# Performance work log

Measured on AMD Instinct MI355X. Metric: run time of the kernel, lower is better.

The kernel has to match this reference:

```python
import jax, jax.numpy as jnp
import numpy as np

K = 20  # top-K neighbors per stock
SLOPE = 0.2  # LeakyReLU negative slope


def _gru_layer(x, Wih, Whh, bih, bhh):
    # x: [N, T, D]; PyTorch GRU gate order: r, z, n
    H = Whh.shape[1]
    def step(h, xt):
        gi = xt @ Wih.T + bih            # [N, 3H]
        gh = h @ Whh.T + bhh             # [N, 3H]
        ir, iz, inn = jnp.split(gi, 3, axis=1)
        hr, hz, hn = jnp.split(gh, 3, axis=1)
        r = jax.nn.sigmoid(ir + hr)
        z = jax.nn.sigmoid(iz + hz)
        n = jnp.tanh(inn + r * hn)
        h_new = (1.0 - z) * n + z * h
        return h_new, h_new
    h0 = jnp.zeros((x.shape[0], H), x.dtype)
    _, ys = jax.lax.scan(step, h0, jnp.swapaxes(x, 0, 1))
    return jnp.swapaxes(ys, 0, 1)        # [N, T, H]


def _cos_sim(x, y):
    # torch: xy / (||x|| ||y||^T), NaN (0/0) replaced by 0
    xy = x @ y.T
    xn = jnp.sqrt(jnp.sum(x * x, axis=1, keepdims=True))
    yn = jnp.sqrt(jnp.sum(y * y, axis=1, keepdims=True))
    denom = xn @ yn.T
    safe = jnp.where(denom == 0.0, 1.0, denom)
    return jnp.where(denom == 0.0, 0.0, xy / safe)


def setup_inputs() -> dict:
    key = jax.random.key(0)
    ks = jax.random.split(key, 20)
    N, T, F, H = 4096, 64, 32, 128
    def rn(k, shape, scale=0.1):
        return jax.random.normal(k, shape, dtype=jnp.float32) * scale
    b01 = lambda n: jnp.full((n,), 0.1, jnp.float32)
    return {
        'x': jax.random.normal(ks[0], (N, T, F), dtype=jnp.float32),
        'Wih0': rn(ks[1], (3 * H, F)), 'Whh0': rn(ks[2], (3 * H, H)),
        'bih0': rn(ks[3], (3 * H,)), 'bhh0': rn(ks[4], (3 * H,)),
        'Wih1': rn(ks[5], (3 * H, H)), 'Whh1': rn(ks[6], (3 * H, H)),
        'bih1': rn(ks[7], (3 * H,)), 'bhh1': rn(ks[8], (3 * H,)),
        'W_hc': rn(ks[9], (H, H)), 'b_hc': b01(H),
        'W_hs': rn(ks[10], (H, H)), 'b_hs': b01(H),
        'W_fore': rn(ks[11], (H, H)), 'b_fore': b01(H),
        'W_back': rn(ks[12], (H, H)), 'b_back': b01(H),
        'W_indi': rn(ks[13], (H, H)), 'b_indi': b01(H),
        'W_out': rn(ks[14], (1, H)), 'b_out': b01(1),
    }


def reference(x, Wih0, Whh0, bih0, bhh0, Wih1, Whh1, bih1, bhh1,
              W_hc, b_hc, W_hs, b_hs, W_fore, b_fore, W_back, b_back,
              W_indi, b_indi, W_out, b_out):
    lrelu = lambda v: jax.nn.leaky_relu(v, SLOPE)
    h = _gru_layer(x, Wih0, Whh0, bih0, bhh0)
    h = _gru_layer(h, Wih1, Whh1, bih1, bhh1)
    g = h[:, -1, :]                                   # [N, H] last-step GRU output
    N = g.shape[0]

    sim = _cos_sim(g, g)                              # [N, N]
    diag = jnp.diagonal(sim)
    sim_off = sim * (1.0 - jnp.eye(N, dtype=sim.dtype))

    # top-K (by |sim|) neighbor mask via scatter
    cols = jax.lax.top_k(jnp.abs(sim_off), K)[1]      # [N, K]
    rows = jnp.repeat(jnp.arange(N), K)
    mask = jnp.zeros((N, N), sim.dtype).at[rows, cols.reshape(-1)].set(1.0)

    tks = sim_off * mask
    col_nz = (jnp.sum(tks, axis=0) != 0).astype(sim.dtype)
    tks = tks + jnp.diag(col_nz * diag)

    # concept features; zero rows (empty concepts) are masked instead of filtered
    concept_raw = tks.T @ g                           # [N, H]
    valid = (jnp.sum(concept_raw, axis=1) != 0).astype(g.dtype)
    cf = lrelu(concept_raw @ W_hc.T + b_hc) * valid[:, None]

    attn = jax.nn.softmax(_cos_sim(g, cf), axis=0)    # softmax over stocks per concept
    hs = lrelu((attn @ cf) @ W_hs.T + b_hs)
    back = lrelu(hs @ W_back.T + b_back)
    fore = lrelu(hs @ W_fore.T + b_fore)
    indi = lrelu((g - back) @ W_indi.T + b_indi)
    pred = (fore + indi) @ W_out.T + b_out            # [N, 1]
    return pred.squeeze(-1)
```

## Files before the change

kernel.cpp:

```cpp
#include <hip/hip_runtime.h>


typedef float f32x4 __attribute__((ext_vector_type(4)));
typedef short s16x8 __attribute__((ext_vector_type(8)));
typedef unsigned short u16;
typedef unsigned long long u64;

#define DEVFN static __device__ __forceinline__

DEVFN u16 f2bf(float f) {
  union { float f; unsigned u; } v; v.f = f;
  return (u16)((v.u + 0x7FFFu + ((v.u >> 16) & 1u)) >> 16);
}

DEVFN f32x4 mfma16(s16x8 a, s16x8 b, f32x4 c) {
  return __builtin_amdgcn_mfma_f32_16x16x32_bf16(a, b, c, 0, 0, 0);
}

DEVFN float sigmf(float x) { return __builtin_amdgcn_rcpf(1.f + __expf(-x)); }
DEVFN float tanhf_fast(float x) {
  float e = __expf(2.f * x);
  return 1.f - 2.f * __builtin_amdgcn_rcpf(e + 1.f);
}
DEVFN float lrelu(float v) { return v > 0.f ? v : 0.2f * v; }

__global__ void cvt_all(const float* __restrict__ w0, const float* __restrict__ w1,
                        const float* __restrict__ w2, const float* __restrict__ w3,
                        const float* __restrict__ w4, const float* __restrict__ w5,
                        const float* __restrict__ w6, const float* __restrict__ w7,
                        u16* __restrict__ dst) {
  int i = blockIdx.x * 256 + threadIdx.x;
  if (i >= 225280) return;
  float v;
  if      (i < 12288)  v = w0[i];
  else if (i < 61440)  v = w1[i - 12288];
  else if (i < 110592) v = w2[i - 61440];
  else if (i < 159744) v = w3[i - 110592];
  else if (i < 176128) v = w4[i - 159744];
  else if (i < 192512) v = w5[i - 176128];
  else if (i < 208896) v = w6[i - 192512];
  else                 v = w7[i - 208896];
  dst[i] = f2bf(v);
}

template<int LAYER>
__launch_bounds__(512, 1)
__global__ void gru_kernel(const void* __restrict__ xin,
                           const u16* __restrict__ Wih, const u16* __restrict__ Whh,
                           const float* __restrict__ bih, const float* __restrict__ bhh,
                           u16* __restrict__ hseq_out, float* __restrict__ g_out)
{
  constexpr int KIN = (LAYER == 0) ? 32 : 128;
  constexpr int NKK = KIN / 32;
  constexpr int XS  = (LAYER == 0) ? 40 : 136;
  const int tid  = threadIdx.x;
  const int w    = tid >> 6;
  const int l    = tid & 63;
  const int quad = l >> 4;
  const int l16  = l & 15;
  const int r0   = blockIdx.x * 16;
  const int c    = w * 16 + l16;

  __shared__ u16 sh_x[16 * XS];
  __shared__ u16 sh_hb[16 * 136];

  s16x8 Bih[3][NKK];
  s16x8 Bhh[3][4];
  float bi[3], bh[3];
#pragma unroll
  for (int g = 0; g < 3; ++g) {
    int j = g * 128 + c;
    bi[g] = bih[j];
    bh[g] = bhh[j];
#pragma unroll
    for (int kk = 0; kk < NKK; ++kk)
      Bih[g][kk] = *(const s16x8*)(Wih + j * KIN + kk * 32 + quad * 8);
#pragma unroll
    for (int kk = 0; kk < 4; ++kk)
      Bhh[g][kk] = *(const s16x8*)(Whh + j * 128 + kk * 32 + quad * 8);
  }
  float hreg[4] = {0.f, 0.f, 0.f, 0.f};
  for (int idx = tid; idx < 16 * 136; idx += 512) sh_hb[idx] = 0;

  for (int t = 0; t < 64; ++t) {
    if constexpr (LAYER == 0) {
      int r = tid >> 5, cc = tid & 31;
      float xv = ((const float*)xin)[(size_t)(r0 + r) * (64 * 32) + t * 32 + cc];
      sh_x[r * XS + cc] = f2bf(xv);
    } else {
      int r = tid >> 5, c4 = (tid & 31) * 4;
      *(ushort4*)(sh_x + r * XS + c4) =
        *(const ushort4*)((const u16*)xin + (size_t)(r0 + r) * (64 * 128) + t * 128 + c4);
    }
    __syncthreads();
    s16x8 ax[NKK], ah[4];
#pragma unroll
    for (int kk = 0; kk < NKK; ++kk)
      ax[kk] = *(const s16x8*)(sh_x + l16 * XS + kk * 32 + quad * 8);
#pragma unroll
    for (int kk = 0; kk < 4; ++kk)
      ah[kk] = *(const s16x8*)(sh_hb + l16 * 136 + kk * 32 + quad * 8);
    __syncthreads();

    f32x4 ai[3], ahh[3];
    const f32x4 zz4 = {0.f, 0.f, 0.f, 0.f};
#pragma unroll
    for (int g = 0; g < 3; ++g) { ai[g] = zz4; ahh[g] = zz4; }
#pragma unroll
    for (int g = 0; g < 3; ++g)
#pragma unroll
      for (int kk = 0; kk < NKK; ++kk) ai[g] = mfma16(ax[kk], Bih[g][kk], ai[g]);
#pragma unroll
    for (int g = 0; g < 3; ++g)
#pragma unroll
      for (int kk = 0; kk < 4; ++kk)  ahh[g] = mfma16(ah[kk], Bhh[g][kk], ahh[g]);

#pragma unroll
    for (int i = 0; i < 4; ++i) {
      int m = quad * 4 + i;
      float rr = sigmf(ai[0][i] + bi[0] + ahh[0][i] + bh[0]);
      float zg = sigmf(ai[1][i] + bi[1] + ahh[1][i] + bh[1]);
      float nn = tanhf_fast(ai[2][i] + bi[2] + rr * (ahh[2][i] + bh[2]));
      float hnew = (1.f - zg) * nn + zg * hreg[i];
      hreg[i] = hnew;
      u16 hb = f2bf(hnew);
      sh_hb[m * 136 + c] = hb;
      if constexpr (LAYER == 0) {
        hseq_out[(size_t)(r0 + m) * (64 * 128) + t * 128 + c] = hb;
      } else {
        if (t == 63) g_out[(size_t)(r0 + m) * 128 + c] = hnew;
      }
    }
  }
}

__global__ void norm_cvt(const float* __restrict__ src, u16* __restrict__ dst,
                         float* __restrict__ rn)
{
  const int tid = threadIdx.x;
  const int wv = tid >> 6, l = tid & 63;
  const int row = blockIdx.x * 4 + wv;
  float2 f2 = *(const float2*)(src + (size_t)row * 128 + l * 2);
  float s = f2.x * f2.x + f2.y * f2.y;
#pragma unroll
  for (int off = 32; off >= 1; off >>= 1) s += __shfl_xor(s, off);
  ushort2 p; p.x = f2bf(f2.x); p.y = f2bf(f2.y);
  *(ushort2*)(dst + (size_t)row * 128 + l * 2) = p;
  if (l == 0) rn[row] = (s == 0.f) ? 0.f : rsqrtf(s);
}

template<int MODE>
__launch_bounds__(256, 1)
__global__ void cos_gemm(const u16* __restrict__ A, const u16* __restrict__ B,
                         const float* __restrict__ rnA, const float* __restrict__ rnB,
                         float* __restrict__ C, u16* __restrict__ E,
                         float* __restrict__ colsum)
{
  __shared__ u16 shA[128 * 136];
  __shared__ u16 shB[128 * 136];
  const int tid = threadIdx.x;
  const int l = tid & 63, wv = tid >> 6;
  const int quad = l >> 4, l16 = l & 15;
  const int i0 = blockIdx.y * 128, j0 = blockIdx.x * 128;
  {
    int r = tid >> 1, half = tid & 1;
    const int4* sa = (const int4*)(A + (size_t)(i0 + r) * 128 + half * 64);
    int4* da = (int4*)(shA + r * 136 + half * 64);
    const int4* sb = (const int4*)(B + (size_t)(j0 + r) * 128 + half * 64);
    int4* db = (int4*)(shB + r * 136 + half * 64);
#pragma unroll
    for (int q = 0; q < 8; ++q) { da[q] = sa[q]; db[q] = sb[q]; }
  }
  __syncthreads();
  const int wm = wv >> 1, wn = wv & 1;
  f32x4 acc[4][4];
  const f32x4 zz4 = {0.f, 0.f, 0.f, 0.f};
#pragma unroll
  for (int a = 0; a < 4; ++a)
#pragma unroll
    for (int b = 0; b < 4; ++b) acc[a][b] = zz4;
#pragma unroll
  for (int kk = 0; kk < 4; ++kk) {
    s16x8 af[4], bfr[4];
#pragma unroll
    for (int mt = 0; mt < 4; ++mt)
      af[mt] = *(const s16x8*)(shA + (wm * 64 + mt * 16 + l16) * 136 + kk * 32 + quad * 8);
#pragma unroll
    for (int nt = 0; nt < 4; ++nt)
      bfr[nt] = *(const s16x8*)(shB + (wn * 64 + nt * 16 + l16) * 136 + kk * 32 + quad * 8);
#pragma unroll
    for (int mt = 0; mt < 4; ++mt)
#pragma unroll
      for (int nt = 0; nt < 4; ++nt) acc[mt][nt] = mfma16(af[mt], bfr[nt], acc[mt][nt]);
  }
  float ra[4][4];
#pragma unroll
  for (int mt = 0; mt < 4; ++mt)
#pragma unroll
    for (int i = 0; i < 4; ++i) ra[mt][i] = rnA[i0 + wm * 64 + mt * 16 + quad * 4 + i];
#pragma unroll
  for (int nt = 0; nt < 4; ++nt) {
    int col = j0 + wn * 64 + nt * 16 + l16;
    float rb = rnB[col];
    float psum = 0.f;
#pragma unroll
    for (int mt = 0; mt < 4; ++mt)
#pragma unroll
      for (int i = 0; i < 4; ++i) {
        int row = i0 + wm * 64 + mt * 16 + quad * 4 + i;
        float v = acc[mt][nt][i] * ra[mt][i] * rb;
        if constexpr (MODE == 0) {
          C[(size_t)row * 4096 + col] = v;
        } else {
          float e = __expf(v);
          E[(size_t)row * 4096 + col] = f2bf(e);
          psum += e;
        }
      }
    if constexpr (MODE == 1) {
      psum += __shfl_xor(psum, 16);
      psum += __shfl_xor(psum, 32);
      if (quad == 0) atomicAdd(colsum + col, psum);
    }
  }
}

__launch_bounds__(256, 1)
__global__ void topk_select(const float* __restrict__ sim,
                            int* __restrict__ gselj, float* __restrict__ gselv,
                            int* __restrict__ cnt, int* __restrict__ touched)
{
  __shared__ unsigned hist[2048];
  __shared__ u64 cand[3072];
  __shared__ int selj[20];
  __shared__ unsigned ws4[4];
  __shared__ int shb, shcnt;
  const int tid = threadIdx.x;
  const int row = blockIdx.x;
  const int l = tid & 63, wv = tid >> 6;

  for (int i = tid; i < 2048; i += 256) hist[i] = 0;
  if (tid == 0) shcnt = 0;
  __syncthreads();

  unsigned key[4][4];
#pragma unroll
  for (int q = 0; q < 4; ++q) {
    int e0 = (q * 256 + tid) * 4;
    float4 v = *(const float4*)(sim + (size_t)row * 4096 + e0);
    key[q][0] = (e0 + 0 == row) ? 0u : (__float_as_uint(v.x) & 0x7FFFFFFFu);
    key[q][1] = (e0 + 1 == row) ? 0u : (__float_as_uint(v.y) & 0x7FFFFFFFu);
    key[q][2] = (e0 + 2 == row) ? 0u : (__float_as_uint(v.z) & 0x7FFFFFFFu);
    key[q][3] = (e0 + 3 == row) ? 0u : (__float_as_uint(v.w) & 0x7FFFFFFFu);
#pragma unroll
    for (int c = 0; c < 4; ++c) {
      unsigned bin = key[q][c] >> 19; if (bin > 2047u) bin = 2047u;
      atomicAdd(&hist[bin], 1u);
    }
  }
  __syncthreads();

  unsigned s = 0;
#pragma unroll
  for (int j = 0; j < 8; ++j) s += hist[tid * 8 + j];
  unsigned r = s;
#pragma unroll
  for (int off = 1; off < 64; off <<= 1) {
    unsigned o = __shfl_down(r, off);
    if (l + off < 64) r += o;
  }
  if (l == 0) ws4[wv] = r;
  __syncthreads();
  unsigned upper = 0;
  for (int q = wv + 1; q < 4; ++q) upper += ws4[q];
  unsigned excl = upper + (r - s);
  if (excl < 20u && excl + s >= 20u) {
    unsigned cum = excl;
    for (int j = 7; j >= 0; --j) {
      cum += hist[tid * 8 + j];
      if (cum >= 20u) { shb = tid * 8 + j; break; }
    }
  }
  __syncthreads();
  const unsigned b = (unsigned)shb;

#pragma unroll
  for (int q = 0; q < 4; ++q) {
    int e0 = (q * 256 + tid) * 4;
#pragma unroll
    for (int c = 0; c < 4; ++c) {
      unsigned bin = key[q][c] >> 19; if (bin > 2047u) bin = 2047u;
      if (bin >= b) {
        int p = atomicAdd(&shcnt, 1);
        if (p < 3072) cand[p] = ((u64)key[q][c] << 32) | (u64)(4095 - (e0 + c));
      }
    }
  }
  __syncthreads();
  const int C = (shcnt < 3072) ? shcnt : 3072;

  if (wv == 0) {
    for (int it = 0; it < 20; ++it) {
      u64 best = 0ull; int bpos = -1;
      for (int p = l; p < C; p += 64) {
        u64 cv = cand[p];
        if (cv > best) { best = cv; bpos = p; }
      }
      u64 mine = best;
#pragma unroll
      for (int off = 1; off < 64; off <<= 1) {
        u64 o = __shfl_xor(best, off);
        if (o > best) best = o;
      }
      if (mine == best && bpos >= 0 && best != 0ull) cand[bpos] = 0ull;
      if (l == 0) selj[it] = 4095 - (int)(best & 0xFFFull);
    }
  }
  __syncthreads();
  if (tid < 20) {
    int idx = selj[tid];
    float sv = (idx == row) ? 0.f : sim[(size_t)row * 4096 + idx];
    gselj[row * 20 + tid] = idx;
    gselv[row * 20 + tid] = sv;
    atomicAdd(&cnt[idx], 1);
    if (sv != 0.f) atomicOr(touched + idx, 1);
  }
}

__launch_bounds__(1024, 1)
__global__ void scan4096(const int* __restrict__ cnt, int* __restrict__ offs,
                         int* __restrict__ cur)
{
  __shared__ int wsum[16];
  const int t = threadIdx.x, l = t & 63, wv = t >> 6;
  int4 c = ((const int4*)cnt)[t];
  int s = c.x + c.y + c.z + c.w;
  int ps = s;
#pragma unroll
  for (int off = 1; off < 64; off <<= 1) {
    int o = __shfl_up(ps, off);
    if (l >= off) ps += o;
  }
  if (l == 63) wsum[wv] = ps;
  __syncthreads();
  if (t == 0) {
    int a = 0;
#pragma unroll
    for (int q = 0; q < 16; ++q) { int x = wsum[q]; wsum[q] = a; a += x; }
  }
  __syncthreads();
  int base = wsum[wv] + (ps - s);
  int4 o4;
  o4.x = base; o4.y = o4.x + c.x; o4.z = o4.y + c.y; o4.w = o4.z + c.z;
  ((int4*)offs)[t] = o4;
  ((int4*)cur)[t] = o4;
}

__global__ void scatter_entries(const int* __restrict__ gselj, const float* __restrict__ gselv,
                                int* __restrict__ cur, int* __restrict__ eid,
                                float* __restrict__ ev)
{
  unsigned idx = blockIdx.x * 256 + threadIdx.x;
  unsigned row = idx / 20u;
  int j = gselj[idx]; float v = gselv[idx];
  int pos = atomicAdd(&cur[j], 1);
  eid[pos] = (int)row; ev[pos] = v;
}

__launch_bounds__(128, 1)
__global__ void concept_cf(const int* __restrict__ offs, const int* __restrict__ cnt,
                           const int* __restrict__ eid, const float* __restrict__ ev,
                           const float* __restrict__ g, const float* __restrict__ sim,
                           const int* __restrict__ touched,
                           const float* __restrict__ Whc, const float* __restrict__ bhc,
                           float* __restrict__ cf, u16* __restrict__ cfbf,
                           float* __restrict__ rncf)
{
  __shared__ float shc[128];
  __shared__ float red2[2];
  const int j = blockIdx.x, d = threadIdx.x;
  const int l = d & 63, wv = d >> 6;
  const int off = offs[j], n = cnt[j];
  float acc = 0.f;
  for (int p = 0; p < n; ++p) {
    int i = eid[off + p]; float v = ev[off + p];
    acc += v * g[(size_t)i * 128 + d];
  }
  if (touched[j]) acc += sim[(size_t)j * 4097] * g[(size_t)j * 128 + d];
  float s = acc;
#pragma unroll
  for (int o = 32; o >= 1; o >>= 1) s += __shfl_xor(s, o);
  if (l == 0) red2[wv] = s;
  shc[d] = acc;
  __syncthreads();
  float valid = ((red2[0] + red2[1]) != 0.f) ? 1.f : 0.f;
  float o = bhc[d];
  const float4* wr = (const float4*)(Whc + (size_t)d * 128);
#pragma unroll 8
  for (int q = 0; q < 32; ++q) {
    float4 w4 = wr[q];
    float4 c4 = *((const float4*)shc + q);
    o += c4.x * w4.x + c4.y * w4.y + c4.z * w4.z + c4.w * w4.w;
  }
  float cfv = lrelu(o) * valid;
  cf[(size_t)j * 128 + d] = cfv;
  cfbf[(size_t)j * 128 + d] = f2bf(cfv);
  __syncthreads();
  float nn = cfv * cfv;
#pragma unroll
  for (int of = 32; of >= 1; of >>= 1) nn += __shfl_xor(nn, of);
  if (l == 0) red2[wv] = nn;
  __syncthreads();
  if (d == 0) {
    float q2 = red2[0] + red2[1];
    rncf[j] = (q2 == 0.f) ? 0.f : rsqrtf(q2);
  }
}

__global__ void scale_cfT(const float* __restrict__ cf, const float* __restrict__ colsum,
                          u16* __restrict__ cfTs)
{
  int idx = blockIdx.x * 256 + threadIdx.x;
  int n = idx >> 12, c = idx & 4095;
  float rz = __builtin_amdgcn_rcpf(colsum[c]);
  cfTs[idx] = f2bf(cf[(size_t)c * 128 + n] * rz);
}

__launch_bounds__(256, 1)
__global__ void attn_cf(const u16* __restrict__ attn, const u16* __restrict__ cfT,
                        float* __restrict__ hs_pre)
{
  __shared__ u16 shw[16 * 136];
  const int tid = threadIdx.x;
  const int l = tid & 63, wv = tid >> 6;
  const int quad = l >> 4, l16 = l & 15;
  const int r0 = blockIdx.x * 16;
  f32x4 acc[2];
  const f32x4 zz4 = {0.f, 0.f, 0.f, 0.f};
  acc[0] = zz4; acc[1] = zz4;
  for (int kc = 0; kc < 32; ++kc) {
    if (kc) __syncthreads();
    {
      int r = tid >> 4, seg = tid & 15;
      *(int4*)(shw + r * 136 + seg * 8) =
        *(const int4*)(attn + (size_t)(r0 + r) * 4096 + kc * 128 + seg * 8);
    }
    __syncthreads();
#pragma unroll
    for (int kk = 0; kk < 4; ++kk) {
      s16x8 a = *(const s16x8*)(shw + l16 * 136 + kk * 32 + quad * 8);
#pragma unroll
      for (int nt = 0; nt < 2; ++nt) {
        int n = wv * 32 + nt * 16 + l16;
        s16x8 b = *(const s16x8*)(cfT + (size_t)n * 4096 + kc * 128 + kk * 32 + quad * 8);
        acc[nt] = mfma16(a, b, acc[nt]);
      }
    }
  }
#pragma unroll
  for (int nt = 0; nt < 2; ++nt)
#pragma unroll
    for (int i = 0; i < 4; ++i) {
      int row = r0 + quad * 4 + i;
      int col = wv * 32 + nt * 16 + l16;
      hs_pre[(size_t)row * 128 + col] = acc[nt][i];
    }
}

__launch_bounds__(256, 1)
__global__ void head_kernel(const float* __restrict__ hs_pre, const float* __restrict__ g,
                            const u16* __restrict__ whs, const u16* __restrict__ wfore,
                            const u16* __restrict__ wback, const u16* __restrict__ windi,
                            const float* __restrict__ b_hs, const float* __restrict__ b_fore,
                            const float* __restrict__ b_back, const float* __restrict__ b_indi,
                            const float* __restrict__ W_out, const float* __restrict__ b_out,
                            float* __restrict__ outp)
{
  __shared__ u16 bufin[16 * 136];
  __shared__ u16 bufB[16 * 136];
  __shared__ float bufF[16 * 132];
  __shared__ float shWout[128];
  const int tid = threadIdx.x;
  const int l = tid & 63, wv = tid >> 6;
  const int quad = l >> 4, l16 = l & 15;
  const int r0 = blockIdx.x * 16;
  const f32x4 zz4 = {0.f, 0.f, 0.f, 0.f};

  if (tid < 128) shWout[tid] = W_out[tid];
  for (int idx = tid; idx < 2048; idx += 256) {
    int j = idx >> 7, n = idx & 127;
    bufin[j * 136 + n] = f2bf(hs_pre[(size_t)(r0 + j) * 128 + n]);
  }
  __syncthreads();
  {
    s16x8 a[4];
#pragma unroll
    for (int kk = 0; kk < 4; ++kk)
      a[kk] = *(const s16x8*)(bufin + l16 * 136 + kk * 32 + quad * 8);
    f32x4 acc[2]; acc[0] = zz4; acc[1] = zz4;
#pragma unroll
    for (int nt = 0; nt < 2; ++nt) {
      int n = wv * 32 + nt * 16 + l16;
#pragma unroll
      for (int kk = 0; kk < 4; ++kk)
        acc[nt] = mfma16(a[kk], *(const s16x8*)(whs + n * 128 + kk * 32 + quad * 8), acc[nt]);
    }
#pragma unroll
    for (int nt = 0; nt < 2; ++nt) {
      int n = wv * 32 + nt * 16 + l16;
      float bb = b_hs[n];
#pragma unroll
      for (int i = 0; i < 4; ++i)
        bufB[(quad * 4 + i) * 136 + n] = f2bf(lrelu(acc[nt][i] + bb));
    }
  }
  __syncthreads();
  {
    s16x8 a[4];
#pragma unroll
    for (int kk = 0; kk < 4; ++kk)
      a[kk] = *(const s16x8*)(bufB + l16 * 136 + kk * 32 + quad * 8);
    f32x4 aF[2], aB[2]; aF[0] = zz4; aF[1] = zz4; aB[0] = zz4; aB[1] = zz4;
#pragma unroll
    for (int nt = 0; nt < 2; ++nt) {
      int n = wv * 32 + nt * 16 + l16;
#pragma unroll
      for (int kk = 0; kk < 4; ++kk) {
        aF[nt] = mfma16(a[kk], *(const s16x8*)(wfore + n * 128 + kk * 32 + quad * 8), aF[nt]);
        aB[nt] = mfma16(a[kk], *(const s16x8*)(wback + n * 128 + kk * 32 + quad * 8), aB[nt]);
      }
    }
#pragma unroll
    for (int nt = 0; nt < 2; ++nt) {
      int n = wv * 32 + nt * 16 + l16;
      float bf_ = b_fore[n], bb_ = b_back[n];
#pragma unroll
      for (int i = 0; i < 4; ++i) {
        int m = quad * 4 + i;
        bufF[m * 132 + n] = lrelu(aF[nt][i] + bf_);
        float back = lrelu(aB[nt][i] + bb_);
        float gv = g[(size_t)(r0 + m) * 128 + n];
        bufin[m * 136 + n] = f2bf(gv - back);
      }
    }
  }
  __syncthreads();
  {
    s16x8 a[4];
#pragma unroll
    for (int kk = 0; kk < 4; ++kk)
      a[kk] = *(const s16x8*)(bufin + l16 * 136 + kk * 32 + quad * 8);
    f32x4 acc[2]; acc[0] = zz4; acc[1] = zz4;
#pragma unroll
    for (int nt = 0; nt < 2; ++nt) {
      int n = wv * 32 + nt * 16 + l16;
#pragma unroll
      for (int kk = 0; kk < 4; ++kk)
        acc[nt] = mfma16(a[kk], *(const s16x8*)(windi + n * 128 + kk * 32 + quad * 8), acc[nt]);
    }
#pragma unroll
    for (int nt = 0; nt < 2; ++nt) {
      int n = wv * 32 + nt * 16 + l16;
      float bi_ = b_indi[n];
#pragma unroll
      for (int i = 0; i < 4; ++i)
        bufF[(quad * 4 + i) * 132 + n] += lrelu(acc[nt][i] + bi_);
    }
  }
  __syncthreads();
  if (tid < 16) {
    float s = b_out[0];
    const float* fr = bufF + tid * 132;
    for (int n = 0; n < 128; ++n) s += fr[n] * shWout[n];
    outp[r0 + tid] = s;
  }
}

static const size_t OFF_A       = 0;
static const size_t OFF_ATTN    = 67108864;
static const size_t OFF_G       = 100663296;
static const size_t OFF_GBF     = 102760448;
static const size_t OFF_RNG     = 103809024;
static const size_t OFF_SELJ    = 103825408;
static const size_t OFF_SELV    = 104153088;
static const size_t OFF_EID     = 104480768;
static const size_t OFF_EV      = 104808448;
static const size_t OFF_CNT     = 105136128;
static const size_t OFF_TOUCH   = 105152512;
static const size_t OFF_COLSUM  = 105168896;
static const size_t OFF_OFFS    = 105185280;
static const size_t OFF_CUR     = 105201664;
static const size_t OFF_CF      = 105218048;
static const size_t OFF_CFBF    = 107315200;
static const size_t OFF_CFTS    = 108363776;
static const size_t OFF_RNCF    = 109412352;
static const size_t OFF_HSPRE   = 109428736;
static const size_t OFF_WB      = 111525888;

extern "C" void kernel_launch(void* const* d_in, const int* in_sizes, int n_in,
                              void* d_out, int out_size, void* d_ws, size_t ws_size,
                              hipStream_t stream)
{
  (void)in_sizes; (void)n_in; (void)out_size; (void)ws_size;
  const float* x      = (const float*)d_in[0];
  const float* Wih0   = (const float*)d_in[1];
  const float* Whh0   = (const float*)d_in[2];
  const float* bih0   = (const float*)d_in[3];
  const float* bhh0   = (const float*)d_in[4];
  const float* Wih1   = (const float*)d_in[5];
  const float* Whh1   = (const float*)d_in[6];
  const float* bih1   = (const float*)d_in[7];
  const float* bhh1   = (const float*)d_in[8];
  const float* W_hc   = (const float*)d_in[9];
  const float* b_hc   = (const float*)d_in[10];
  const float* W_hs   = (const float*)d_in[11];
  const float* b_hs   = (const float*)d_in[12];
  const float* W_fore = (const float*)d_in[13];
  const float* b_fore = (const float*)d_in[14];
  const float* W_back = (const float*)d_in[15];
  const float* b_back = (const float*)d_in[16];
  const float* W_indi = (const float*)d_in[17];
  const float* b_indi = (const float*)d_in[18];
  const float* W_out  = (const float*)d_in[19];
  const float* b_out  = (const float*)d_in[20];

  char* ws = (char*)d_ws;
  u16*   hseq    = (u16*)(ws + OFF_A);
  float* simbuf  = (float*)(ws + OFF_A);
  u16*   attnb   = (u16*)(ws + OFF_ATTN);
  float* gbuf    = (float*)(ws + OFF_G);
  u16*   gbf     = (u16*)(ws + OFF_GBF);
  float* rng     = (float*)(ws + OFF_RNG);
  int*   gselj   = (int*)(ws + OFF_SELJ);
  float* gselv   = (float*)(ws + OFF_SELV);
  int*   eid     = (int*)(ws + OFF_EID);
  float* ev      = (float*)(ws + OFF_EV);
  int*   cntb    = (int*)(ws + OFF_CNT);
  int*   touched = (int*)(ws + OFF_TOUCH);
  float* colsum  = (float*)(ws + OFF_COLSUM);
  int*   offsb   = (int*)(ws + OFF_OFFS);
  int*   curb    = (int*)(ws + OFF_CUR);
  float* cf      = (float*)(ws + OFF_CF);
  u16*   cfbf    = (u16*)(ws + OFF_CFBF);
  u16*   cfTs    = (u16*)(ws + OFF_CFTS);
  float* rncf    = (float*)(ws + OFF_RNCF);
  float* hs_pre  = (float*)(ws + OFF_HSPRE);
  u16*   wsB     = (u16*)(ws + OFF_WB);
  u16 *wih0b = wsB, *whh0b = wsB + 12288, *wih1b = wsB + 61440, *whh1b = wsB + 110592;
  u16 *whsb = wsB + 159744, *wforeb = wsB + 176128, *wbackb = wsB + 192512, *windib = wsB + 208896;

  cvt_all<<<880, 256, 0, stream>>>(Wih0, Whh0, Wih1, Whh1, W_hs, W_fore, W_back, W_indi, wsB);

  gru_kernel<0><<<256, 512, 0, stream>>>((const void*)x, wih0b, whh0b, bih0, bhh0,
                                         hseq, (float*)nullptr);
  gru_kernel<1><<<256, 512, 0, stream>>>((const void*)hseq, wih1b, whh1b, bih1, bhh1,
                                         (u16*)nullptr, gbuf);

  norm_cvt<<<1024, 256, 0, stream>>>(gbuf, gbf, rng);
  cos_gemm<0><<<dim3(32, 32), 256, 0, stream>>>(gbf, gbf, rng, rng, simbuf,
                                                (u16*)nullptr, (float*)nullptr);

  hipMemsetAsync(ws + OFF_CNT, 0, 49152, stream);
  topk_select<<<4096, 256, 0, stream>>>(simbuf, gselj, gselv, cntb, touched);
  scan4096<<<1, 1024, 0, stream>>>(cntb, offsb, curb);
  scatter_entries<<<320, 256, 0, stream>>>(gselj, gselv, curb, eid, ev);
  concept_cf<<<4096, 128, 0, stream>>>(offsb, cntb, eid, ev, gbuf, simbuf, touched,
                                       W_hc, b_hc, cf, cfbf, rncf);

  cos_gemm<1><<<dim3(32, 32), 256, 0, stream>>>(gbf, cfbf, rng, rncf, (float*)nullptr,
                                                attnb, colsum);
  scale_cfT<<<2048, 256, 0, stream>>>(cf, colsum, cfTs);
  attn_cf<<<256, 256, 0, stream>>>(attnb, cfTs, hs_pre);

  head_kernel<<<256, 256, 0, stream>>>(hs_pre, gbuf, whsb, wforeb, wbackb, windib,
                                       b_hs, b_fore, b_back, b_indi, W_out, b_out,
                                       (float*)d_out);
}
```

Baseline: 499.0 us.

## Fuse both GRU layers into one kernel with double-buffered hidden state

Merges the two per-layer GRU kernels into one kernel that runs layer 0 and layer 1 in lockstep per timestep. The layer-0 hidden sequence is no longer written to and re-read from global memory, and one launch goes away. Shared hidden-state buffers are double-buffered to save a barrier, and the next x slice is prefetched into a register. In exchange, each thread holds all four weight sets in registers (higher VGPR pressure under launch_bounds 512,2), and the serial dependency chain per step gets longer.

After: 444.5 us. -10.9%, faster.

```diff
diff --git a/kernel.cpp b/kernel.cpp
--- a/kernel.cpp
+++ b/kernel.cpp
@@ -43,16 +43,14 @@
   dst[i] = f2bf(v);
 }
 
-template<int LAYER>
-__launch_bounds__(512, 1)
-__global__ void gru_kernel(const void* __restrict__ xin,
-                           const u16* __restrict__ Wih, const u16* __restrict__ Whh,
-                           const float* __restrict__ bih, const float* __restrict__ bhh,
-                           u16* __restrict__ hseq_out, float* __restrict__ g_out)
-{
-  constexpr int KIN = (LAYER == 0) ? 32 : 128;
-  constexpr int NKK = KIN / 32;
-  constexpr int XS  = (LAYER == 0) ? 40 : 136;
+__launch_bounds__(512, 2)
+__global__ void gru_fused(const float* __restrict__ x,
+                          const u16* __restrict__ Wih0, const u16* __restrict__ Whh0,
+                          const float* __restrict__ bih0, const float* __restrict__ bhh0,
+                          const u16* __restrict__ Wih1, const u16* __restrict__ Whh1,
+                          const float* __restrict__ bih1, const float* __restrict__ bhh1,
+                          float* __restrict__ g_out)
+{
   const int tid  = threadIdx.x;
   const int w    = tid >> 6;
   const int l    = tid & 63;
@@ -61,73 +59,95 @@
   const int r0   = blockIdx.x * 16;
   const int c    = w * 16 + l16;
 
-  __shared__ u16 sh_x[16 * XS];
-  __shared__ u16 sh_hb[16 * 136];
-
-  s16x8 Bih[3][NKK];
-  s16x8 Bhh[3][4];
-  float bi[3], bh[3];
+  __shared__ u16 sh_x[16 * 40];
+  __shared__ u16 sh_h0[2][16 * 136];
+  __shared__ u16 sh_h1[2][16 * 136];
+
+  s16x8 B0ih[3];
+  s16x8 B0hh[3][4];
+  s16x8 B1ih[3][4];
+  s16x8 B1hh[3][4];
+  float bi0[3], bh0[3], bi1[3], bh1[3];
 #pragma unroll
   for (int g = 0; g < 3; ++g) {
     int j = g * 128 + c;
-    bi[g] = bih[j];
-    bh[g] = bhh[j];
-#pragma unroll
-    for (int kk = 0; kk < NKK; ++kk)
-      Bih[g][kk] = *(const s16x8*)(Wih + j * KIN + kk * 32 + quad * 8);
-#pragma unroll
-    for (int kk = 0; kk < 4; ++kk)
-      Bhh[g][kk] = *(const s16x8*)(Whh + j * 128 + kk * 32 + quad * 8);
-  }
-  float hreg[4] = {0.f, 0.f, 0.f, 0.f};
-  for (int idx = tid; idx < 16 * 136; idx += 512) sh_hb[idx] = 0;
-
+    bi0[g] = bih0[j]; bh0[g] = bhh0[j];
+    bi1[g] = bih1[j]; bh1[g] = bhh1[j];
+    B0ih[g] = *(const s16x8*)(Wih0 + j * 32 + quad * 8);
+#pragma unroll
+    for (int kk = 0; kk < 4; ++kk) {
+      B0hh[g][kk] = *(const s16x8*)(Whh0 + j * 128 + kk * 32 + quad * 8);
+      B1ih[g][kk] = *(const s16x8*)(Wih1 + j * 128 + kk * 32 + quad * 8);
+      B1hh[g][kk] = *(const s16x8*)(Whh1 + j * 128 + kk * 32 + quad * 8);
+    }
+  }
+  float h0reg[4] = {0.f, 0.f, 0.f, 0.f};
+  float h1reg[4] = {0.f, 0.f, 0.f, 0.f};
+  for (int idx = tid; idx < 16 * 136; idx += 512) {
+    sh_h0[0][idx] = 0; sh_h1[0][idx] = 0;
+  }
+  const int xr = tid >> 5, xc = tid & 31;
+  float xpre = x[(size_t)(r0 + xr) * 2048 + xc];
+  __syncthreads();
+
+  const f32x4 zz4 = {0.f, 0.f, 0.f, 0.f};
   for (int t = 0; t < 64; ++t) {
-    if constexpr (LAYER == 0) {
-      int r = tid >> 5, cc = tid & 31;
-      float xv = ((const float*)xin)[(size_t)(r0 + r) * (64 * 32) + t * 32 + cc];
-      sh_x[r * XS + cc] = f2bf(xv);
-    } else {
-      int r = tid >> 5, c4 = (tid & 31) * 4;
-      *(ushort4*)(sh_x + r * XS + c4) =
-        *(const ushort4*)((const u16*)xin + (size_t)(r0 + r) * (64 * 128) + t * 128 + c4);
-    }
+    const int cur = t & 1, nxt = cur ^ 1;
+    sh_x[xr * 40 + xc] = f2bf(xpre);
     __syncthreads();
-    s16x8 ax[NKK], ah[4];
-#pragma unroll
-    for (int kk = 0; kk < NKK; ++kk)
-      ax[kk] = *(const s16x8*)(sh_x + l16 * XS + kk * 32 + quad * 8);
-#pragma unroll
-    for (int kk = 0; kk < 4; ++kk)
-      ah[kk] = *(const s16x8*)(sh_hb + l16 * 136 + kk * 32 + quad * 8);
+    s16x8 ax = *(const s16x8*)(sh_x + l16 * 40 + quad * 8);
+    s16x8 ah0[4], ah1[4];
+#pragma unroll
+    for (int kk = 0; kk < 4; ++kk) {
+      ah0[kk] = *(const s16x8*)(sh_h0[cur] + l16 * 136 + kk * 32 + quad * 8);
+      ah1[kk] = *(const s16x8*)(sh_h1[cur] + l16 * 136 + kk * 32 + quad * 8);
+    }
+    if (t < 63) xpre = x[(size_t)(r0 + xr) * 2048 + (t + 1) * 32 + xc];
+
+    {
+      f32x4 ai[3], ah[3];
+#pragma unroll
+      for (int g = 0; g < 3; ++g) { ai[g] = mfma16(ax, B0ih[g], zz4); ah[g] = zz4; }
+#pragma unroll
+      for (int g = 0; g < 3; ++g)
+#pragma unroll
+        for (int kk = 0; kk < 4; ++kk) ah[g] = mfma16(ah0[kk], B0hh[g][kk], ah[g]);
+#pragma unroll
+      for (int i = 0; i < 4; ++i) {
+        int m = quad * 4 + i;
+        float rr = sigmf(ai[0][i] + bi0[0] + ah[0][i] + bh0[0]);
+        float zg = sigmf(ai[1][i] + bi0[1] + ah[1][i] + bh0[1]);
+        float nn = tanhf_fast(ai[2][i] + bi0[2] + rr * (ah[2][i] + bh0[2]));
+        float hnew = (1.f - zg) * nn + zg * h0reg[i];
+        h0reg[i] = hnew;
+        sh_h0[nxt][m * 136 + c] = f2bf(hnew);
+      }
+    }
     __syncthreads();
-
-    f32x4 ai[3], ahh[3];
-    const f32x4 zz4 = {0.f, 0.f, 0.f, 0.f};
-#pragma unroll
-    for (int g = 0; g < 3; ++g) { ai[g] = zz4; ahh[g] = zz4; }
-#pragma unroll
-    for (int g = 0; g < 3; ++g)
-#pragma unroll
-      for (int kk = 0; kk < NKK; ++kk) ai[g] = mfma16(ax[kk], Bih[g][kk], ai[g]);
-#pragma unroll
-    for (int g = 0; g < 3; ++g)
-#pragma unroll
-      for (int kk = 0; kk < 4; ++kk)  ahh[g] = mfma16(ah[kk], Bhh[g][kk], ahh[g]);
-
-#pragma unroll
-    for (int i = 0; i < 4; ++i) {
-      int m = quad * 4 + i;
-      float rr = sigmf(ai[0][i] + bi[0] + ahh[0][i] + bh[0]);
-      float zg = sigmf(ai[1][i] + bi[1] + ahh[1][i] + bh[1]);
-      float nn = tanhf_fast(ai[2][i] + bi[2] + rr * (ahh[2][i] + bh[2]));
-      float hnew = (1.f - zg) * nn + zg * hreg[i];
-      hreg[i] = hnew;
-      u16 hb = f2bf(hnew);
-      sh_hb[m * 136 + c] = hb;
-      if constexpr (LAYER == 0) {
-        hseq_out[(size_t)(r0 + m) * (64 * 128) + t * 128 + c] = hb;
-      } else {
+    {
+      s16x8 a1x[4];
+#pragma unroll
+      for (int kk = 0; kk < 4; ++kk)
+        a1x[kk] = *(const s16x8*)(sh_h0[nxt] + l16 * 136 + kk * 32 + quad * 8);
+      f32x4 ai[3], ah[3];
+#pragma unroll
+      for (int g = 0; g < 3; ++g) { ai[g] = zz4; ah[g] = zz4; }
+#pragma unroll
+      for (int g = 0; g < 3; ++g)
+#pragma unroll
+        for (int kk = 0; kk < 4; ++kk) {
+          ai[g] = mfma16(a1x[kk], B1ih[g][kk], ai[g]);
+          ah[g] = mfma16(ah1[kk], B1hh[g][kk], ah[g]);
+        }
+#pragma unroll
+      for (int i = 0; i < 4; ++i) {
+        int m = quad * 4 + i;
+        float rr = sigmf(ai[0][i] + bi1[0] + ah[0][i] + bh1[0]);
+        float zg = sigmf(ai[1][i] + bi1[1] + ah[1][i] + bh1[1]);
+        float nn = tanhf_fast(ai[2][i] + bi1[2] + rr * (ah[2][i] + bh1[2]));
+        float hnew = (1.f - zg) * nn + zg * h1reg[i];
+        h1reg[i] = hnew;
+        sh_h1[nxt][m * 136 + c] = f2bf(hnew);
         if (t == 63) g_out[(size_t)(r0 + m) * 128 + c] = hnew;
       }
     }
@@ -625,7 +645,6 @@
   const float* b_out  = (const float*)d_in[20];
 
   char* ws = (char*)d_ws;
-  u16*   hseq    = (u16*)(ws + OFF_A);
   float* simbuf  = (float*)(ws + OFF_A);
   u16*   attnb   = (u16*)(ws + OFF_ATTN);
   float* gbuf    = (float*)(ws + OFF_G);
@@ -651,10 +670,8 @@
 
   cvt_all<<<880, 256, 0, stream>>>(Wih0, Whh0, Wih1, Whh1, W_hs, W_fore, W_back, W_indi, wsB);
 
-  gru_kernel<0><<<256, 512, 0, stream>>>((const void*)x, wih0b, whh0b, bih0, bhh0,
-                                         hseq, (float*)nullptr);
-  gru_kernel<1><<<256, 512, 0, stream>>>((const void*)hseq, wih1b, whh1b, bih1, bhh1,
-                                         (u16*)nullptr, gbuf);
+  gru_fused<<<256, 512, 0, stream>>>(x, wih0b, whh0b, bih0, bhh0,
+                                     wih1b, whh1b, bih1, bhh1, gbuf);
 
   norm_cvt<<<1024, 256, 0, stream>>>(gbuf, gbf, rng);
   cos_gemm<0><<<dim3(32, 32), 256, 0, stream>>>(gbf, gbf, rng, rng, simbuf,
```
